# Kernel optimization log

Measured on AMD Instinct MI355X. Metric: run time of the kernel, lower is better.

The kernel has to match this reference:

```python
import jax, jax.numpy as jnp
import numpy as np

B, S, D = 1, 2048, 2048
H, G, HD = 32, 8, 64        # n_heads, n_kv_groups, head_dim
GS = H // G                  # group_size
ROPE_BASE = 10000.0


def _rope_tables(seq_len, head_dim):
    inv_freq = 1.0 / (ROPE_BASE ** (jnp.arange(0, head_dim, 2, dtype=jnp.float32) / head_dim))
    angles = jnp.arange(seq_len, dtype=jnp.float32)[:, None] * inv_freq[None, :]  # [S, HD/2]
    angles = jnp.concatenate([angles, angles], axis=-1)                            # [S, HD]
    return jnp.cos(angles), jnp.sin(angles)


def setup_inputs() -> dict:
    key = jax.random.key(0)
    ks = jax.random.split(key, 5)
    x = jax.random.normal(ks[0], (B, S, D), dtype=jnp.float32)
    mask = jnp.triu(jnp.ones((S, S), dtype=bool), k=1)  # True = masked (causal)
    cos_vals, sin_vals = _rope_tables(S, HD)
    scale = 0.02
    Wq = jax.random.normal(ks[1], (H * HD, D), dtype=jnp.float32) * scale
    Wk = jax.random.normal(ks[2], (G * HD, D), dtype=jnp.float32) * scale
    Wv = jax.random.normal(ks[3], (G * HD, D), dtype=jnp.float32) * scale
    Wo = jax.random.normal(ks[4], (D, H * HD), dtype=jnp.float32) * scale
    return {"x": x, "mask": mask, "cos_vals": cos_vals, "sin_vals": sin_vals,
            "Wq": Wq, "Wk": Wk, "Wv": Wv, "Wo": Wo}


def _apply_rope(t, cos, sin):
    # t: [b, heads, S, HD]; cos/sin: [S, HD]
    half = t.shape[-1] // 2
    t1, t2 = t[..., :half], t[..., half:]
    rotated = jnp.concatenate([-t2, t1], axis=-1)
    return t * cos[None, None] + rotated * sin[None, None]


def reference(x, mask, cos_vals, sin_vals, Wq, Wk, Wv, Wo):
    b, s, _ = x.shape
    q = (x @ Wq.T).reshape(b, s, H, HD).transpose(0, 2, 1, 3)   # [b,H,S,HD]
    k = (x @ Wk.T).reshape(b, s, G, HD).transpose(0, 2, 1, 3)   # [b,G,S,HD]
    v = (x @ Wv.T).reshape(b, s, G, HD).transpose(0, 2, 1, 3)   # [b,G,S,HD]
    q = _apply_rope(q, cos_vals, sin_vals)
    k = _apply_rope(k, cos_vals, sin_vals)
    # Group-broadcast instead of repeat_interleave (same math)
    q = q.reshape(b, G, GS, s, HD)
    scores = jnp.einsum('bghqd,bgkd->bghqk', q, k)              # [b,G,GS,S,S]
    scores = jnp.where(mask[None, None, None], -jnp.inf, scores)
    weights = jax.nn.softmax(scores / np.sqrt(HD).astype(np.float32), axis=-1)
    out = jnp.einsum('bghqk,bgkd->bghqd', weights, v)           # [b,G,GS,S,HD]
    out = out.reshape(b, H, s, HD).transpose(0, 2, 1, 3).reshape(b, s, H * HD)
    return out @ Wo.T
```

## Files before the change

### kernel.cpp

```cpp
#include <hip/hip_runtime.h>
#include <cstddef>
#include <cstdint>

#define S 2048
#define Dm 2048
#define NH 32
#define NG 8
#define HD 64

typedef __attribute__((ext_vector_type(8))) short bf16x8;
typedef __attribute__((ext_vector_type(4))) short bf16x4;
typedef __attribute__((ext_vector_type(4))) float f32x4;

__device__ __forceinline__ float fast_exp2(float x) { return __builtin_amdgcn_exp2f(x); }

__device__ __forceinline__ unsigned short f2bf(float f) {
  unsigned int u = __builtin_bit_cast(unsigned int, f);
  u = (u + 0x7fffu + ((u >> 16) & 1u)) >> 16;
  return (unsigned short)u;
}
__device__ __forceinline__ unsigned int pk2bf(float lo, float hi) {
  unsigned int a = __builtin_bit_cast(unsigned int, lo) + 0x8000u;
  unsigned int b = __builtin_bit_cast(unsigned int, hi) + 0x8000u;
  return (a >> 16) | (b & 0xffff0000u);
}
__device__ __forceinline__ void gl_lds16(const unsigned short* g, unsigned short* l) {
  __builtin_amdgcn_global_load_lds(
      (const __attribute__((address_space(1))) unsigned int*)g,
      (__attribute__((address_space(3))) unsigned int*)l, 16, 0, 0);
}

#define QSC 0.1803368801111601f

__global__ __launch_bounds__(256) void cvt_all(const float* __restrict__ x,
                                               const float* __restrict__ Wq,
                                               const float* __restrict__ Wk,
                                               const float* __restrict__ Wv,
                                               const float* __restrict__ Wo,
                                               unsigned short* __restrict__ xb,
                                               unsigned short* __restrict__ Wcat,
                                               unsigned short* __restrict__ Wob) {
  int i = blockIdx.x * 256 + threadIdx.x;
  const float4* src;
  ushort4* dst;
  if (i < 1048576)      { src = (const float4*)x  + i;             dst = (ushort4*)xb + i; }
  else if (i < 2097152) { src = (const float4*)Wq + (i - 1048576); dst = (ushort4*)Wcat + (i - 1048576); }
  else if (i < 2359296) { src = (const float4*)Wk + (i - 2097152); dst = (ushort4*)Wcat + 1048576 + (i - 2097152); }
  else if (i < 2621440) { src = (const float4*)Wv + (i - 2359296); dst = (ushort4*)Wcat + 1310720 + (i - 2359296); }
  else                  { src = (const float4*)Wo + (i - 2621440); dst = (ushort4*)Wob + (i - 2621440); }
  float4 v = *src;
  ushort4 o;
  o.x = f2bf(v.x); o.y = f2bf(v.y); o.z = f2bf(v.z); o.w = f2bf(v.w);
  *dst = o;
}

__global__ __launch_bounds__(256) void gemm_bf16(const unsigned short* __restrict__ A,
                                                 const unsigned short* __restrict__ B,
                                                 float* __restrict__ Cf,
                                                 unsigned short* __restrict__ Cb,
                                                 unsigned short* __restrict__ VtOut,
                                                 const float* __restrict__ cosv,
                                                 const float* __restrict__ sinv,
                                                 int M, int N, int K) {
  __shared__ __align__(16) unsigned short As[3][64 * 64];
  __shared__ __align__(16) unsigned short Bs[3][128 * 64];
  const int tid = threadIdx.x;
  const int lane = tid & 63, wave = tid >> 6;
  const int row0 = blockIdx.y * 64, col0 = blockIdx.x * 128;
  const int wr = (wave >> 1) * 32, wc = (wave & 1) * 64;

  f32x4 acc[2][4];
#pragma unroll
  for (int i = 0; i < 2; i++)
#pragma unroll
    for (int j = 0; j < 4; j++) acc[i][j] = (f32x4){0.f, 0.f, 0.f, 0.f};

  const int arow0 = tid >> 3, aslot0 = ((tid & 7) ^ (arow0 & 7)) * 8;
  const int arow1 = (tid + 256) >> 3, aslot1 = (((tid + 256) & 7) ^ (arow1 & 7)) * 8;
  const int fr = lane & 15, q4 = lane >> 4;

  int brow[4], bslot[4];
#pragma unroll
  for (int b = 0; b < 4; b++) {
    int p = tid + b * 256;
    brow[b] = p >> 3;
    bslot[b] = ((p & 7) ^ (brow[b] & 7)) * 8;
  }

  const int nk = K >> 6;

  auto stage = [&](int k0, int buf) {
    gl_lds16(&A[(size_t)(row0 + arow0) * K + k0 + aslot0], &As[buf][tid * 8]);
    gl_lds16(&A[(size_t)(row0 + arow1) * K + k0 + aslot1], &As[buf][(tid + 256) * 8]);
#pragma unroll
    for (int b = 0; b < 4; b++)
      gl_lds16(&B[(size_t)(col0 + brow[b]) * K + k0 + bslot[b]], &Bs[buf][(tid + b * 256) * 8]);
  };

  stage(0, 0);
  stage(64, 1);

  int cur = 0;
  for (int t = 0; t < nk; ++t) {
    if (t + 1 < nk) asm volatile("s_waitcnt vmcnt(6)" ::: "memory");
    else            asm volatile("s_waitcnt vmcnt(0)" ::: "memory");
    asm volatile("s_barrier" ::: "memory");

    if (t + 2 < nk) {
      int sb = cur + 2; if (sb >= 3) sb -= 3;
      stage((t + 2) << 6, sb);
    }

    const unsigned short* Ab = As[cur];
    const unsigned short* Bb = Bs[cur];
#pragma unroll
    for (int kk = 0; kk < 2; kk++) {
      bf16x8 af[2], bfr[4];
#pragma unroll
      for (int i = 0; i < 2; i++) {
        int R = wr + i * 16 + fr;
        af[i] = *(const bf16x8*)&Ab[R * 64 + ((q4 + kk * 4) ^ (R & 7)) * 8];
      }
#pragma unroll
      for (int j = 0; j < 4; j++) {
        int R = wc + j * 16 + fr;
        bfr[j] = *(const bf16x8*)&Bb[R * 64 + ((q4 + kk * 4) ^ (R & 7)) * 8];
      }
#pragma unroll
      for (int i = 0; i < 2; i++)
#pragma unroll
        for (int j = 0; j < 4; j++)
          acc[i][j] = __builtin_amdgcn_mfma_f32_16x16x32_bf16(af[i], bfr[j], acc[i][j], 0, 0, 0);
    }

    cur = cur + 1; if (cur == 3) cur = 0;
  }

  const int cc = lane & 15, cr = (lane >> 4) * 4;

  if (cosv) {
#pragma unroll
    for (int i = 0; i < 2; i++) {
      int grb = row0 + wr + i * 16 + cr;
#pragma unroll
      for (int j = 0; j < 2; j++) {
        int gc = col0 + wc + j * 16 + cc;
        if (gc < 2560) {
          int d = j * 16 + cc;
          float qs = (gc < 2048) ? QSC : 1.0f;
#pragma unroll
          for (int r = 0; r < 4; r++) {
            float c = cosv[(grb + r) * 64 + d];
            float s = sinv[(grb + r) * 64 + d];
            float t1 = acc[i][j][r], t2 = acc[i][j + 2][r];
            acc[i][j][r]     = (t1 * c - t2 * s) * qs;
            acc[i][j + 2][r] = (t2 * c + t1 * s) * qs;
          }
        }
      }
    }
  }

#pragma unroll
  for (int i = 0; i < 2; i++)
#pragma unroll
    for (int j = 0; j < 4; j++) {
      int gc = col0 + wc + j * 16 + cc;
#pragma unroll
      for (int r = 0; r < 4; r++) {
        int gr = row0 + wr + i * 16 + cr + r;
        if (cosv) {
          if (gc >= 2560) VtOut[(size_t)(gc - 2560) * 2048 + gr] = f2bf(acc[i][j][r]);
          else            Cb[(size_t)gr * N + gc] = f2bf(acc[i][j][r]);
        } else if (Cf)    Cf[(size_t)gr * N + gc] = acc[i][j][r];
        else              Cb[(size_t)gr * N + gc] = f2bf(acc[i][j][r]);
      }
    }
}

__global__ __launch_bounds__(256, 2) void flash_mfma(const unsigned short* __restrict__ QKV,
                                                     const unsigned short* __restrict__ Vt_g,
                                                     unsigned short* __restrict__ Ob) {
  __shared__ __align__(16) unsigned short Ks[2][64 * 64];
  __shared__ __align__(16) unsigned short Vs[2][64 * 64];

  const int tid = threadIdx.x;
  const int lane = tid & 63, wave = tid >> 6;
  const int m15 = lane & 15, q4 = lane >> 4;

  const int L = blockIdx.x;
  const int h = L & 31, g = h >> 2;
  const int u0 = L >> 5, a = u0 >> 3, b = u0 & 7;
  const int u = (a == 0) ? 15 - b : b;
  const int qb = u * 128;
  const int ntiles = 2 * u + 2;

  bf16x8 qf[2][2];
#pragma unroll
  for (int f = 0; f < 2; f++) {
    const size_t qrow = (size_t)(qb + f * 64 + wave * 16 + m15) * 3072 + h * 64;
    qf[f][0] = *(const bf16x8*)&QKV[qrow + q4 * 8];
    qf[f][1] = *(const bf16x8*)&QKV[qrow + 32 + q4 * 8];
  }

  f32x4 accO[2][4];
  float l_lane[2] = {0.f, 0.f};
#pragma unroll
  for (int f = 0; f < 2; f++)
#pragma unroll
    for (int v = 0; v < 4; v++) accO[f][v] = (f32x4){0.f, 0.f, 0.f, 0.f};

  const int p0 = wave * 128 + lane, p1 = p0 + 64;
  const int sr0 = p0 >> 3, so0 = ((p0 & 7) ^ (sr0 & 7)) * 8;
  const int sr1 = p1 >> 3, so1 = ((p1 & 7) ^ (sr1 & 7)) * 8;

#pragma unroll
  for (int t = 0; t < 2; t++) {
    const int k0 = t * 64;
    gl_lds16(&QKV[(size_t)(k0 + sr0) * 3072 + 2048 + g * 64 + so0], &Ks[t][p0 * 8]);
    gl_lds16(&QKV[(size_t)(k0 + sr1) * 3072 + 2048 + g * 64 + so1], &Ks[t][p1 * 8]);
    gl_lds16(&Vt_g[(size_t)(g * 64 + sr0) * 2048 + k0 + so0], &Vs[t][p0 * 8]);
    gl_lds16(&Vt_g[(size_t)(g * 64 + sr1) * 2048 + k0 + so1], &Vs[t][p1 * 8]);
  }

  for (int t = 0; t < ntiles; t++) {
    if (t + 1 < ntiles) asm volatile("s_waitcnt vmcnt(4)" ::: "memory");
    else                asm volatile("s_waitcnt vmcnt(0)" ::: "memory");
    asm volatile("s_barrier" ::: "memory");

    const unsigned short* Kb = Ks[t & 1];
    const unsigned short* Vb = Vs[t & 1];
    const bool act0 = (t < ntiles - 1);

    f32x4 sc[2][4];
#pragma unroll
    for (int kt = 0; kt < 4; kt++) {
      const int krow = kt * 16 + m15;
      bf16x8 kf0 = *(const bf16x8*)&Kb[krow * 64 + (q4 ^ (krow & 7)) * 8];
      bf16x8 kf1 = *(const bf16x8*)&Kb[krow * 64 + ((q4 + 4) ^ (krow & 7)) * 8];
      f32x4 z1 = (f32x4){0.f, 0.f, 0.f, 0.f};
      z1 = __builtin_amdgcn_mfma_f32_16x16x32_bf16(kf0, qf[1][0], z1, 0, 0, 0);
      sc[1][kt] = __builtin_amdgcn_mfma_f32_16x16x32_bf16(kf1, qf[1][1], z1, 0, 0, 0);
      if (act0) {
        f32x4 z0 = (f32x4){0.f, 0.f, 0.f, 0.f};
        z0 = __builtin_amdgcn_mfma_f32_16x16x32_bf16(kf0, qf[0][0], z0, 0, 0, 0);
        sc[0][kt] = __builtin_amdgcn_mfma_f32_16x16x32_bf16(kf1, qf[0][1], z0, 0, 0, 0);
      }
    }

    bf16x8 pA0[2], pA1[2];
#pragma unroll
    for (int f = 0; f < 2; f++) {
      if (f == 0 && !act0) continue;
      if (t == 2 * u + f) {
        const int qo = wave * 16 + m15;
#pragma unroll
        for (int kt = 0; kt < 4; kt++)
#pragma unroll
          for (int r = 0; r < 4; r++)
            if (kt * 16 + q4 * 4 + r > qo) sc[f][kt][r] = -1e30f;
      }
      float rs = 0.f;
#pragma unroll
      for (int kt = 0; kt < 4; kt++)
#pragma unroll
        for (int r = 0; r < 4; r++) {
          float p = fast_exp2(sc[f][kt][r]);
          sc[f][kt][r] = p;
          rs += p;
        }
      l_lane[f] += rs;

      int4 pa0, pa1;
      pa0.x = pk2bf(sc[f][0][0], sc[f][0][1]); pa0.y = pk2bf(sc[f][0][2], sc[f][0][3]);
      pa0.z = pk2bf(sc[f][1][0], sc[f][1][1]); pa0.w = pk2bf(sc[f][1][2], sc[f][1][3]);
      pa1.x = pk2bf(sc[f][2][0], sc[f][2][1]); pa1.y = pk2bf(sc[f][2][2], sc[f][2][3]);
      pa1.z = pk2bf(sc[f][3][0], sc[f][3][1]); pa1.w = pk2bf(sc[f][3][2], sc[f][3][3]);
      pA0[f] = __builtin_bit_cast(bf16x8, pa0);
      pA1[f] = __builtin_bit_cast(bf16x8, pa1);
    }

#pragma unroll
    for (int vt = 0; vt < 4; vt++) {
      const int vrow = vt * 16 + m15;
      const int base = vrow * 64, sw = vrow & 7, half = (q4 & 1) * 4, c1 = q4 >> 1;
      bf16x4 w00 = *(const bf16x4*)&Vb[base + (c1 ^ sw) * 8 + half];
      bf16x4 w01 = *(const bf16x4*)&Vb[base + ((c1 + 2) ^ sw) * 8 + half];
      bf16x4 w10 = *(const bf16x4*)&Vb[base + ((c1 + 4) ^ sw) * 8 + half];
      bf16x4 w11 = *(const bf16x4*)&Vb[base + ((c1 + 6) ^ sw) * 8 + half];
      bf16x8 vB0 = __builtin_shufflevector(w00, w01, 0, 1, 2, 3, 4, 5, 6, 7);
      bf16x8 vB1 = __builtin_shufflevector(w10, w11, 0, 1, 2, 3, 4, 5, 6, 7);
      accO[1][vt] = __builtin_amdgcn_mfma_f32_16x16x32_bf16(pA0[1], vB0, accO[1][vt], 0, 0, 0);
      accO[1][vt] = __builtin_amdgcn_mfma_f32_16x16x32_bf16(pA1[1], vB1, accO[1][vt], 0, 0, 0);
      if (act0) {
        accO[0][vt] = __builtin_amdgcn_mfma_f32_16x16x32_bf16(pA0[0], vB0, accO[0][vt], 0, 0, 0);
        accO[0][vt] = __builtin_amdgcn_mfma_f32_16x16x32_bf16(pA1[0], vB1, accO[0][vt], 0, 0, 0);
      }
    }

    asm volatile("s_barrier" ::: "memory");
    if (t + 2 < ntiles) {
      const int k2 = (t + 2) * 64;
      unsigned short* Kn = (unsigned short*)Ks[t & 1];
      unsigned short* Vn = (unsigned short*)Vs[t & 1];
      gl_lds16(&QKV[(size_t)(k2 + sr0) * 3072 + 2048 + g * 64 + so0], &Kn[p0 * 8]);
      gl_lds16(&QKV[(size_t)(k2 + sr1) * 3072 + 2048 + g * 64 + so1], &Kn[p1 * 8]);
      gl_lds16(&Vt_g[(size_t)(g * 64 + sr0) * 2048 + k2 + so0], &Vn[p0 * 8]);
      gl_lds16(&Vt_g[(size_t)(g * 64 + sr1) * 2048 + k2 + so1], &Vn[p1 * 8]);
    }
  }

#pragma unroll
  for (int f = 0; f < 2; f++) {
    float lsum = l_lane[f];
    lsum += __shfl_xor(lsum, 16);
    lsum += __shfl_xor(lsum, 32);
    float lr[4];
#pragma unroll
    for (int r = 0; r < 4; r++) lr[r] = 1.0f / __shfl(lsum, q4 * 20 + r);
#pragma unroll
    for (int vt = 0; vt < 4; vt++)
#pragma unroll
      for (int r = 0; r < 4; r++) {
        int row = qb + f * 64 + wave * 16 + q4 * 4 + r;
        Ob[(size_t)row * 2048 + h * 64 + vt * 16 + m15] = f2bf(accO[f][vt][r] * lr[r]);
      }
  }
}

extern "C" void kernel_launch(void* const* d_in, const int* in_sizes, int n_in,
                              void* d_out, int out_size, void* d_ws, size_t ws_size,
                              hipStream_t stream) {
  const float* x    = (const float*)d_in[0];
  const float* cosv = (const float*)d_in[2];
  const float* sinv = (const float*)d_in[3];
  const float* Wq   = (const float*)d_in[4];
  const float* Wk   = (const float*)d_in[5];
  const float* Wv   = (const float*)d_in[6];
  const float* Wo   = (const float*)d_in[7];
  float* out = (float*)d_out;

  unsigned short* xb   = (unsigned short*)d_ws;
  unsigned short* Wcat = xb + (size_t)2048 * 2048;
  unsigned short* Wob  = Wcat + (size_t)3072 * 2048;
  unsigned short* QKV  = Wob + (size_t)2048 * 2048;
  unsigned short* Vt_g = QKV + (size_t)3072 * 2048;

  dim3 blk(256);
  cvt_all<<<14336, blk, 0, stream>>>(x, Wq, Wk, Wv, Wo, xb, Wcat, Wob);
  gemm_bf16<<<dim3(24, 32), blk, 0, stream>>>(xb, Wcat, nullptr, QKV, Vt_g, cosv, sinv, 2048, 3072, 2048);
  flash_mfma<<<512, blk, 0, stream>>>(QKV, Vt_g, xb);
  gemm_bf16<<<dim3(16, 32), blk, 0, stream>>>(xb, Wob, out, nullptr, nullptr, nullptr, nullptr, 2048, 2048, 2048);
}
```

Baseline: 241.9 us.

## Template GEMM tile height, enlarge QKV tiles, switch to double-buffered staging

The GEMM is templated on the M tile count. The QKV projection now uses 128x128 tiles (MI=4), giving half as many blocks and more reuse per block, while the output projection keeps 64x128. LDS staging drops from a triple buffer to a double buffer: the next tile is issued only after compute and a lgkmcnt drain plus barrier, which may expose more load latency. The flash kernel's barrier before restaging also gains an explicit LDS drain.

After: 230.0 us. -4.9%, faster.

```diff
diff --git a/kernel.cpp b/kernel.cpp
--- a/kernel.cpp
+++ b/kernel.cpp
@@ -28,6 +28,11 @@
   __builtin_amdgcn_global_load_lds(
       (const __attribute__((address_space(1))) unsigned int*)g,
       (__attribute__((address_space(3))) unsigned int*)l, 16, 0, 0);
+}
+
+__device__ __forceinline__ void lds_drain_barrier() {
+  asm volatile("s_waitcnt lgkmcnt(0)" ::: "memory");
+  asm volatile("s_barrier" ::: "memory");
 }
 
 #define QSC 0.1803368801111601f
@@ -54,6 +59,7 @@
   *dst = o;
 }
 
+template<int MI>
 __global__ __launch_bounds__(256) void gemm_bf16(const unsigned short* __restrict__ A,
                                                  const unsigned short* __restrict__ B,
                                                  float* __restrict__ Cf,
@@ -62,62 +68,44 @@
                                                  const float* __restrict__ cosv,
                                                  const float* __restrict__ sinv,
                                                  int M, int N, int K) {
-  __shared__ __align__(16) unsigned short As[3][64 * 64];
-  __shared__ __align__(16) unsigned short Bs[3][128 * 64];
+  constexpr int BM = MI * 32;
+  __shared__ __align__(16) unsigned short As[2][BM * 64];
+  __shared__ __align__(16) unsigned short Bs[2][128 * 64];
   const int tid = threadIdx.x;
   const int lane = tid & 63, wave = tid >> 6;
-  const int row0 = blockIdx.y * 64, col0 = blockIdx.x * 128;
-  const int wr = (wave >> 1) * 32, wc = (wave & 1) * 64;
-
-  f32x4 acc[2][4];
-#pragma unroll
-  for (int i = 0; i < 2; i++)
+  const int row0 = blockIdx.y * BM, col0 = blockIdx.x * 128;
+  const int wr = (wave >> 1) * (MI * 16), wc = (wave & 1) * 64;
+  const int fr = lane & 15, q4 = lane >> 4;
+
+  f32x4 acc[MI][4];
+#pragma unroll
+  for (int i = 0; i < MI; i++)
 #pragma unroll
     for (int j = 0; j < 4; j++) acc[i][j] = (f32x4){0.f, 0.f, 0.f, 0.f};
 
-  const int arow0 = tid >> 3, aslot0 = ((tid & 7) ^ (arow0 & 7)) * 8;
-  const int arow1 = (tid + 256) >> 3, aslot1 = (((tid + 256) & 7) ^ (arow1 & 7)) * 8;
-  const int fr = lane & 15, q4 = lane >> 4;
-
-  int brow[4], bslot[4];
-#pragma unroll
-  for (int b = 0; b < 4; b++) {
-    int p = tid + b * 256;
-    brow[b] = p >> 3;
-    bslot[b] = ((p & 7) ^ (brow[b] & 7)) * 8;
-  }
-
   const int nk = K >> 6;
 
   auto stage = [&](int k0, int buf) {
-    gl_lds16(&A[(size_t)(row0 + arow0) * K + k0 + aslot0], &As[buf][tid * 8]);
-    gl_lds16(&A[(size_t)(row0 + arow1) * K + k0 + aslot1], &As[buf][(tid + 256) * 8]);
-#pragma unroll
-    for (int b = 0; b < 4; b++)
-      gl_lds16(&B[(size_t)(col0 + brow[b]) * K + k0 + bslot[b]], &Bs[buf][(tid + b * 256) * 8]);
+#pragma unroll
+    for (int c = 0; c < MI; c++) {
+      int p = tid + c * 256;
+      int r = p >> 3, sl = ((p & 7) ^ (r & 7)) * 8;
+      gl_lds16(&A[(size_t)(row0 + r) * K + k0 + sl], &As[buf][p * 8]);
+    }
+#pragma unroll
+    for (int b = 0; b < 4; b++) {
+      int p = tid + b * 256;
+      int r = p >> 3, sl = ((p & 7) ^ (r & 7)) * 8;
+      gl_lds16(&B[(size_t)(col0 + r) * K + k0 + sl], &Bs[buf][p * 8]);
+    }
   };
 
-  stage(0, 0);
-  stage(64, 1);
-
-  int cur = 0;
-  for (int t = 0; t < nk; ++t) {
-    if (t + 1 < nk) asm volatile("s_waitcnt vmcnt(6)" ::: "memory");
-    else            asm volatile("s_waitcnt vmcnt(0)" ::: "memory");
-    asm volatile("s_barrier" ::: "memory");
-
-    if (t + 2 < nk) {
-      int sb = cur + 2; if (sb >= 3) sb -= 3;
-      stage((t + 2) << 6, sb);
-    }
-
-    const unsigned short* Ab = As[cur];
-    const unsigned short* Bb = Bs[cur];
+  auto compute = [&](const unsigned short* Ab, const unsigned short* Bb) {
 #pragma unroll
     for (int kk = 0; kk < 2; kk++) {
-      bf16x8 af[2], bfr[4];
-#pragma unroll
-      for (int i = 0; i < 2; i++) {
+      bf16x8 af[MI], bfr[4];
+#pragma unroll
+      for (int i = 0; i < MI; i++) {
         int R = wr + i * 16 + fr;
         af[i] = *(const bf16x8*)&Ab[R * 64 + ((q4 + kk * 4) ^ (R & 7)) * 8];
       }
@@ -127,20 +115,36 @@
         bfr[j] = *(const bf16x8*)&Bb[R * 64 + ((q4 + kk * 4) ^ (R & 7)) * 8];
       }
 #pragma unroll
-      for (int i = 0; i < 2; i++)
+      for (int i = 0; i < MI; i++)
 #pragma unroll
         for (int j = 0; j < 4; j++)
           acc[i][j] = __builtin_amdgcn_mfma_f32_16x16x32_bf16(af[i], bfr[j], acc[i][j], 0, 0, 0);
     }
-
-    cur = cur + 1; if (cur == 3) cur = 0;
+  };
+
+  stage(0, 0);
+  stage(64, 1);
+
+  for (int t = 0; t < nk; ++t) {
+    if (t + 1 < nk) {
+      if constexpr (MI == 2) asm volatile("s_waitcnt vmcnt(6)" ::: "memory");
+      else                   asm volatile("s_waitcnt vmcnt(8)" ::: "memory");
+    } else {
+      asm volatile("s_waitcnt vmcnt(0)" ::: "memory");
+    }
+    asm volatile("s_barrier" ::: "memory");
+
+    compute(As[t & 1], Bs[t & 1]);
+
+    lds_drain_barrier();
+    if (t + 2 < nk) stage((t + 2) << 6, t & 1);
   }
 
   const int cc = lane & 15, cr = (lane >> 4) * 4;
 
   if (cosv) {
 #pragma unroll
-    for (int i = 0; i < 2; i++) {
+    for (int i = 0; i < MI; i++) {
       int grb = row0 + wr + i * 16 + cr;
 #pragma unroll
       for (int j = 0; j < 2; j++) {
@@ -162,7 +166,7 @@
   }
 
 #pragma unroll
-  for (int i = 0; i < 2; i++)
+  for (int i = 0; i < MI; i++)
 #pragma unroll
     for (int j = 0; j < 4; j++) {
       int gc = col0 + wc + j * 16 + cc;
@@ -298,7 +302,7 @@
       }
     }
 
-    asm volatile("s_barrier" ::: "memory");
+    lds_drain_barrier();
     if (t + 2 < ntiles) {
       const int k2 = (t + 2) * 64;
       unsigned short* Kn = (unsigned short*)Ks[t & 1];
@@ -348,7 +352,7 @@
 
   dim3 blk(256);
   cvt_all<<<14336, blk, 0, stream>>>(x, Wq, Wk, Wv, Wo, xb, Wcat, Wob);
-  gemm_bf16<<<dim3(24, 32), blk, 0, stream>>>(xb, Wcat, nullptr, QKV, Vt_g, cosv, sinv, 2048, 3072, 2048);
+  gemm_bf16<4><<<dim3(24, 16), blk, 0, stream>>>(xb, Wcat, nullptr, QKV, Vt_g, cosv, sinv, 2048, 3072, 2048);
   flash_mfma<<<512, blk, 0, stream>>>(QKV, Vt_g, xb);
-  gemm_bf16<<<dim3(16, 32), blk, 0, stream>>>(xb, Wob, out, nullptr, nullptr, nullptr, nullptr, 2048, 2048, 2048);
-}
+  gemm_bf16<2><<<dim3(16, 32), blk, 0, stream>>>(xb, Wob, out, nullptr, nullptr, nullptr, nullptr, 2048, 2048, 2048);
+}
```
